# Performance work log

Measured on AMD Instinct MI355X. Metric: run time of the kernel, lower is better.

Reference implementation:

```python
import jax, jax.numpy as jnp
import numpy as np

N = 100000
E = 500000
D_IN = 128
D_H = 128
MAX_ITERS = 3  # min(int(T=2.0)+1, 3); step weights all >= 0.5 so no early break


def setup_inputs() -> dict:
    key = jax.random.key(0)
    ks = jax.random.split(key, 7)
    node_feats = jax.random.normal(ks[0], (N, D_IN), dtype=jnp.float32)
    edge_index = jax.random.randint(ks[1], (2, E), 0, N, dtype=jnp.int64)
    init = lambda k, shp, fan: jax.random.normal(k, shp, dtype=jnp.float32) / np.float32(np.sqrt(fan))
    W_s = init(ks[2], (D_H, D_IN), D_IN)        # Linear(d_in, d_h, bias=False)
    W_pc = init(ks[3], (D_H, D_H), D_H)         # Linear(d_h, d_h, bias=False)
    W_edge = init(ks[4], (D_H, 2 * D_H), 2 * D_H)  # Linear(2*d_h, d_h, bias=False)
    W_gate_w = init(ks[5], (1, 2 * D_H), 2 * D_H)  # Linear(2*d_h, 1)
    W_gate_b = jnp.zeros((1,), jnp.float32)
    T = jnp.float32(2.0)  # learnable iteration-count parameter, init tree_iterations
    return dict(node_feats=node_feats, edge_index=edge_index, W_s=W_s, W_pc=W_pc,
                W_edge=W_edge, W_gate_w=W_gate_w, W_gate_b=W_gate_b, T=T)


def _step(h, p_idx, c_idx, W_pc, W_edge, W_gate_w, W_gate_b):
    h_p = h[p_idx]                                   # [E, d_h] gather
    h_c = h[c_idx]                                   # [E, d_h] gather
    ec = jnp.concatenate([h_p, h_c], axis=1)         # [E, 2*d_h]
    msg = ec @ W_edge.T                              # edge projection
    alpha = jax.nn.sigmoid(ec @ W_gate_w.T + W_gate_b)  # [E, 1] gate
    msg = msg * alpha
    # scatter_add into both endpoints (symmetric aggregation)
    agg = jnp.zeros_like(h).at[p_idx].add(msg).at[c_idx].add(msg)
    new_h = jax.nn.relu(agg @ W_pc.T + h)
    return new_h + h  # residual=True


def reference(node_feats, edge_index, W_s, W_pc, W_edge, W_gate_w, W_gate_b, T):
    p_idx, c_idx = edge_index[0], edge_index[1]
    h = node_feats @ W_s.T                           # [N, d_h]
    for step in range(MAX_ITERS):
        w = jax.nn.sigmoid(T - step)                 # learned step weight
        step_h = _step(h, p_idx, c_idx, W_pc, W_edge, W_gate_w, W_gate_b)
        h = h + w * (step_h - h)
    return h  # outputs['hidden'] (dropout is identity in eval)
```

## Files before the change

### kernel.cpp

```cpp
#include <hip/hip_runtime.h>
#include <cstdio>
#include <cstddef>

#define DH 128

typedef _Float16 f16;
typedef __attribute__((ext_vector_type(8))) _Float16 f16x8;
typedef __attribute__((ext_vector_type(4))) _Float16 f16x4;
typedef __attribute__((ext_vector_type(2))) _Float16 f16x2;
typedef __attribute__((ext_vector_type(4))) float    f32x4;
typedef unsigned int u32;

__global__ __launch_bounds__(128) void wc_kernel(const float* __restrict__ Wpc,
                                                 const float* __restrict__ Wedge,
                                                 const float* __restrict__ Ws,
                                                 f16* __restrict__ Bg16,
                                                 f16* __restrict__ Ws16)
{
    int o = blockIdx.x;
    int k = threadIdx.x;
    if (o < 256) {
        int orow = o & 127;
        int col  = (o < 128) ? k : (128 + k);
        float acc = 0.f;
        for (int m = 0; m < 128; ++m)
            acc += Wpc[orow * 128 + m] * Wedge[m * 256 + col];
        Bg16[o * 128 + k] = (f16)acc;
    } else {
        int row = o - 256;
        Ws16[row * 128 + k] = (f16)Ws[row * 128 + k];
    }
}

__global__ __launch_bounds__(256) void prep_k(const int* __restrict__ idx,
                                              int* __restrict__ cnt, int twoE,
                                              const float* __restrict__ x,
                                              f16* __restrict__ x16, int n4)
{
    const int stride = gridDim.x * blockDim.x;
    const int mx = (twoE > n4) ? twoE : n4;
    for (int i = blockIdx.x * blockDim.x + threadIdx.x; i < mx; i += stride) {
        if (i < twoE) atomicAdd(cnt + idx[i], 1);
        if (i < n4) {
            float4 v = ((const float4*)x)[i];
            f16x2 a = {(f16)v.x, (f16)v.y};
            f16x2 b = {(f16)v.z, (f16)v.w};
            ((f16x2*)x16)[2 * i]     = a;
            ((f16x2*)x16)[2 * i + 1] = b;
        }
    }
}

template<int OUT, bool WF32, bool WF16, bool FUSES>
__global__ __launch_bounds__(256) void mfma_gemm_t(const f16* __restrict__ A16,
                                                   const f16* __restrict__ B16,
                                                   float* __restrict__ Cf,
                                                   f16* __restrict__ Ch,
                                                   const float* __restrict__ wg,
                                                   float* __restrict__ s,
                                                   int M)
{
    const int lane = threadIdx.x & 63;
    const int row0 = blockIdx.x * 128 + (threadIdx.x >> 6) * 32;
    const int r = lane & 15, kg = lane >> 4;

    const int mA = row0 + r,      mB = row0 + 16 + r;
    const bool okA = (mA < M),    okB = (mB < M);
    const int arA = okA ? mA : M - 1, arB = okB ? mB : M - 1;
    const f16x8* ApA = (const f16x8*)(A16 + (size_t)arA * 128 + kg * 8);
    const f16x8* ApB = (const f16x8*)(A16 + (size_t)arB * 128 + kg * 8);
    f16x8 a0 = ApA[0], a1 = ApA[4], a2 = ApA[8], a3 = ApA[12];
    f16x8 e0 = ApB[0], e1 = ApB[4], e2 = ApB[8], e3 = ApB[12];

    float spA0 = 0.f, spA1 = 0.f, spB0 = 0.f, spB1 = 0.f;

    for (int ct = 0; ct < OUT / 16; ++ct) {
        const f16x8* Bp = (const f16x8*)(B16 + (size_t)(ct * 16 + r) * 128 + kg * 8);
        f16x8 b0 = Bp[0], b1 = Bp[4], b2 = Bp[8], b3 = Bp[12];
        f32x4 acc0 = {0.f,0.f,0.f,0.f}, acc1 = {0.f,0.f,0.f,0.f};
        f32x4 acc2 = {0.f,0.f,0.f,0.f}, acc3 = {0.f,0.f,0.f,0.f};
        acc0 = __builtin_amdgcn_mfma_f32_16x16x32_f16(b0, a0, acc0, 0, 0, 0);
        acc2 = __builtin_amdgcn_mfma_f32_16x16x32_f16(b0, e0, acc2, 0, 0, 0);
        acc1 = __builtin_amdgcn_mfma_f32_16x16x32_f16(b2, a2, acc1, 0, 0, 0);
        acc3 = __builtin_amdgcn_mfma_f32_16x16x32_f16(b2, e2, acc3, 0, 0, 0);
        acc0 = __builtin_amdgcn_mfma_f32_16x16x32_f16(b1, a1, acc0, 0, 0, 0);
        acc2 = __builtin_amdgcn_mfma_f32_16x16x32_f16(b1, e1, acc2, 0, 0, 0);
        acc1 = __builtin_amdgcn_mfma_f32_16x16x32_f16(b3, a3, acc1, 0, 0, 0);
        acc3 = __builtin_amdgcn_mfma_f32_16x16x32_f16(b3, e3, acc3, 0, 0, 0);

        const int o0 = ct * 16 + kg * 4;
        float vA0 = acc0[0]+acc1[0], vA1 = acc0[1]+acc1[1];
        float vA2 = acc0[2]+acc1[2], vA3 = acc0[3]+acc1[3];
        float vB0 = acc2[0]+acc3[0], vB1 = acc2[1]+acc3[1];
        float vB2 = acc2[2]+acc3[2], vB3 = acc2[3]+acc3[3];
        if (okA) {
            if constexpr (WF32)
                *(float4*)(Cf + (size_t)mA * OUT + o0) = make_float4(vA0, vA1, vA2, vA3);
            if constexpr (WF16) {
                f16x4 hv = {(f16)vA0, (f16)vA1, (f16)vA2, (f16)vA3};
                *(f16x4*)(Ch + (size_t)mA * OUT + o0) = hv;
            }
        }
        if (okB) {
            if constexpr (WF32)
                *(float4*)(Cf + (size_t)mB * OUT + o0) = make_float4(vB0, vB1, vB2, vB3);
            if constexpr (WF16) {
                f16x4 hv = {(f16)vB0, (f16)vB1, (f16)vB2, (f16)vB3};
                *(f16x4*)(Ch + (size_t)mB * OUT + o0) = hv;
            }
        }
        if constexpr (FUSES) {
            float w0 = wg[o0], w1 = wg[o0+1], w2 = wg[o0+2], w3 = wg[o0+3];
            float u0 = wg[128+o0], u1 = wg[128+o0+1], u2 = wg[128+o0+2], u3 = wg[128+o0+3];
            spA0 += vA0*w0 + vA1*w1 + vA2*w2 + vA3*w3;
            spA1 += vA0*u0 + vA1*u1 + vA2*u2 + vA3*u3;
            spB0 += vB0*w0 + vB1*w1 + vB2*w2 + vB3*w3;
            spB1 += vB0*u0 + vB1*u1 + vB2*u2 + vB3*u3;
        }
    }
    if constexpr (FUSES) {
        spA0 += __shfl_xor(spA0, 16); spA0 += __shfl_xor(spA0, 32);
        spA1 += __shfl_xor(spA1, 16); spA1 += __shfl_xor(spA1, 32);
        spB0 += __shfl_xor(spB0, 16); spB0 += __shfl_xor(spB0, 32);
        spB1 += __shfl_xor(spB1, 16); spB1 += __shfl_xor(spB1, 32);
        if (kg == 0) {
            if (okA) *(float2*)(s + 2 * mA) = make_float2(spA0, spA1);
            if (okB) *(float2*)(s + 2 * mB) = make_float2(spB0, spB1);
        }
    }
}

#define SCAN_B 256
__global__ __launch_bounds__(SCAN_B) void scan1(const int* __restrict__ cnt,
                                                int* __restrict__ bsum, int Nn)
{
    __shared__ int sm[SCAN_B];
    int i = blockIdx.x * SCAN_B + threadIdx.x;
    sm[threadIdx.x] = (i < Nn) ? cnt[i] : 0;
    __syncthreads();
    for (int off = SCAN_B / 2; off > 0; off >>= 1) {
        if (threadIdx.x < off) sm[threadIdx.x] += sm[threadIdx.x + off];
        __syncthreads();
    }
    if (threadIdx.x == 0) bsum[blockIdx.x] = sm[0];
}

__global__ __launch_bounds__(1024) void scan2(int* __restrict__ bsum, int nb,
                                              int* __restrict__ totalOut)
{
    __shared__ int sm[1024];
    int t = threadIdx.x;
    sm[t] = (t < nb) ? bsum[t] : 0;
    __syncthreads();
    for (int off = 1; off < 1024; off <<= 1) {
        int u = (t >= off) ? sm[t - off] : 0;
        __syncthreads();
        sm[t] += u;
        __syncthreads();
    }
    if (t < nb) bsum[t] = (t == 0) ? 0 : sm[t - 1];
    if (t == nb - 1) *totalOut = sm[t];
}

__global__ __launch_bounds__(SCAN_B) void scan3(const int* __restrict__ cnt,
                                                const int* __restrict__ bsum,
                                                int* __restrict__ base,
                                                int* __restrict__ cursor, int Nn)
{
    __shared__ int sm[SCAN_B];
    int i = blockIdx.x * SCAN_B + threadIdx.x;
    int v = (i < Nn) ? cnt[i] : 0;
    sm[threadIdx.x] = v;
    __syncthreads();
    for (int off = 1; off < SCAN_B; off <<= 1) {
        int u = (threadIdx.x >= off) ? sm[threadIdx.x - off] : 0;
        __syncthreads();
        sm[threadIdx.x] += u;
        __syncthreads();
    }
    if (i < Nn) {
        int b = bsum[blockIdx.x] + sm[threadIdx.x] - v;
        base[i] = b;
        cursor[i] = b;
    }
}

__global__ __launch_bounds__(256) void fill_xcd(const int* __restrict__ idx,
                                                int* __restrict__ cursor,
                                                int* __restrict__ adjp,
                                                int E, int Nn)
{
    const int xcd  = blockIdx.x & 7;
    const int gblk = blockIdx.x >> 3;
    const int ngrp = gridDim.x >> 3;
    const int twoE = 2 * E;
    const int lo = xcd * Nn, hi = lo + Nn;
    for (int i = gblk * blockDim.x + threadIdx.x; i < twoE; i += ngrp * blockDim.x) {
        int node = idx[i];
        int n8 = node << 3;
        if (n8 < lo || n8 >= hi) continue;
        int side  = (i >= E);
        int e     = side ? i - E : i;
        int other = side ? idx[e] : idx[E + e];
        int pos = atomicAdd(cursor + node, 1);
        adjp[pos] = other | (side << 31);
    }
}

template<bool LAST>
__global__ __launch_bounds__(256) void agg4(const f16* __restrict__ g16,
                                            const int* __restrict__ adjp,
                                            const int* __restrict__ base,
                                            const float* __restrict__ sIn,
                                            float* __restrict__ sOut,
                                            float* __restrict__ h,
                                            f16* __restrict__ h16,
                                            const float* __restrict__ wg,
                                            const float* __restrict__ gbp,
                                            const float* __restrict__ Tp,
                                            float stepf, int Nn)
{
    const int lane = threadIdx.x & 63;
    const int n = (blockIdx.x * blockDim.x + threadIdx.x) >> 6;
    if (n >= Nn) return;
    const float gb = gbp[0];
    const float w  = 1.f / (1.f + expf(-(Tp[0] - stepf)));
    const int b0 = base[n], b1 = base[n + 1];
    const float s1n = sIn[2 * n], s2n = sIn[2 * n + 1];
    const int sub = lane >> 5;
    const int d0  = (lane & 31) << 2;

    f16x4 o1 = *(const f16x4*)(g16 + (size_t)n * 256 + d0);
    f16x4 o2 = *(const f16x4*)(g16 + (size_t)n * 256 + 128 + d0);
    float4 hv = *(const float4*)(h + (size_t)n * DH + d0);

    f16x2 accLo = {(f16)0.f, (f16)0.f};
    f16x2 accHi = {(f16)0.f, (f16)0.f};
    float aPl = 0.f, aCl = 0.f;

    union V4 { f16x4 v; f16x2 h2[2]; };
    union AU { u32 w; f16x2 h; unsigned short us[2]; };

    for (int c0 = b0; c0 < b1; c0 += 64) {
        const int m = (b1 - c0 < 64) ? (b1 - c0) : 64;
        int meta = adjp[c0 + ((lane < m) ? lane : (m - 1))];
        int other = meta & 0x7FFFFFFF;
        int side  = ((unsigned)meta) >> 31;
        int eoff  = (other << 8) | ((side ^ 1) << 7);
        float sv  = sIn[2 * other + (side ^ 1)];
        float aE  = 1.f / (1.f + expf(-((side ? s2n : s1n) + sv + gb)));
        if (lane >= m) aE = 0.f;
        aPl += side ? 0.f : aE;
        aCl += side ? aE : 0.f;

        AU apk;
        apk.h[0] = (f16)aE;
        apk.us[1] = apk.us[0];

        for (int j = 0; j < m; j += 16) {
            V4 gv[8]; u32 ap[8];
#pragma unroll
            for (int u = 0; u < 8; ++u) {
                int es = j + 2 * u + sub; es = (es < 63) ? es : 63;
                int eo = __shfl(eoff, es);
                ap[u]  = (u32)__shfl((int)apk.w, es);
                gv[u].v = *(const f16x4*)(g16 + (size_t)(unsigned)eo + d0);
            }
#pragma unroll
            for (int u = 0; u < 8; ++u) {
                AU aa; aa.w = ap[u];
                accLo += aa.h * gv[u].h2[0];
                accHi += aa.h * gv[u].h2[1];
            }
        }
    }

    float ax = (float)accLo[0], ay = (float)accLo[1];
    float az = (float)accHi[0], aw = (float)accHi[1];

    ax += __shfl_xor(ax, 32); ay += __shfl_xor(ay, 32);
    az += __shfl_xor(az, 32); aw += __shfl_xor(aw, 32);
    float aP = aPl, aC = aCl;
#pragma unroll
    for (int off = 32; off > 0; off >>= 1) {
        aP += __shfl_xor(aP, off);
        aC += __shfl_xor(aC, off);
    }
    ax += aP * (float)o1[0] + aC * (float)o2[0];
    ay += aP * (float)o1[1] + aC * (float)o2[1];
    az += aP * (float)o1[2] + aC * (float)o2[2];
    aw += aP * (float)o1[3] + aC * (float)o2[3];

    hv.x += w * fmaxf(ax + hv.x, 0.f);
    hv.y += w * fmaxf(ay + hv.y, 0.f);
    hv.z += w * fmaxf(az + hv.z, 0.f);
    hv.w += w * fmaxf(aw + hv.w, 0.f);

    float p0 = 0.f, p1 = 0.f;
    if (lane < 32) {
        *(float4*)(h + (size_t)n * DH + d0) = hv;
        if constexpr (!LAST) {
            f16x4 h2 = {(f16)hv.x, (f16)hv.y, (f16)hv.z, (f16)hv.w};
            *(f16x4*)(h16 + (size_t)n * DH + d0) = h2;
            float4 w0 = *(const float4*)(wg + d0);
            float4 w1 = *(const float4*)(wg + 128 + d0);
            p0 = hv.x*w0.x + hv.y*w0.y + hv.z*w0.z + hv.w*w0.w;
            p1 = hv.x*w1.x + hv.y*w1.y + hv.z*w1.z + hv.w*w1.w;
        }
    }
    if constexpr (!LAST) {
#pragma unroll
        for (int off = 16; off > 0; off >>= 1) {
            p0 += __shfl_xor(p0, off);
            p1 += __shfl_xor(p1, off);
        }
        if (lane == 0) *(float2*)(sOut + 2 * n) = make_float2(p0, p1);
    }
}

static inline size_t alignUp(size_t x) { return (x + 255) & ~(size_t)255; }

extern "C" void kernel_launch(void* const* d_in, const int* in_sizes, int n_in,
                              void* d_out, int out_size, void* d_ws, size_t ws_size,
                              hipStream_t stream)
{
    const float* x     = (const float*)d_in[0];
    const int*   idx   = (const int*)d_in[1];
    const float* Ws    = (const float*)d_in[2];
    const float* Wpc   = (const float*)d_in[3];
    const float* Wedge = (const float*)d_in[4];
    const float* Wg    = (const float*)d_in[5];
    const float* Wgb   = (const float*)d_in[6];
    const float* Tp    = (const float*)d_in[7];
    const int Nn = in_sizes[0] / DH;
    const int E  = in_sizes[1] / 2;
    float* h = (float*)d_out;

    const int nb = (Nn + SCAN_B - 1) / SCAN_B;
    if (nb > 1024) { fprintf(stderr, "kernel_launch: Nn too big for scan\n"); return; }

    size_t off = 0;
    char* wsb = (char*)d_ws;
    f16*   g16    = (f16*)  (wsb + off); off = alignUp(off + (size_t)Nn * 256 * 2);
    f16*   h16    = (f16*)  (wsb + off); off = alignUp(off + (size_t)Nn * DH * 2);
    f16*   x16    = (f16*)  (wsb + off); off = alignUp(off + (size_t)Nn * DH * 2);
    f16*   Ws16   = (f16*)  (wsb + off); off = alignUp(off + 128 * 128 * 2);
    f16*   Bg16   = (f16*)  (wsb + off); off = alignUp(off + 256 * 128 * 2);
    float* sA     = (float*)(wsb + off); off = alignUp(off + (size_t)Nn * 2 * 4);
    float* sB     = (float*)(wsb + off); off = alignUp(off + (size_t)Nn * 2 * 4);
    int*   cnt    = (int*)  (wsb + off); off = alignUp(off + (size_t)Nn * 4);
    int*   base   = (int*)  (wsb + off); off = alignUp(off + (size_t)(Nn + 1) * 4);
    int*   cursor = (int*)  (wsb + off); off = alignUp(off + (size_t)Nn * 4);
    int*   bsum   = (int*)  (wsb + off); off = alignUp(off + 1024 * 4);
    int*   adjp   = (int*)  (wsb + off); off = alignUp(off + (size_t)(2 * E) * 4);
    if (off > ws_size) {
        fprintf(stderr, "kernel_launch: ws too small (%zu < %zu)\n", ws_size, off);
        return;
    }

    hipMemsetAsync(cnt, 0, (size_t)Nn * 4, stream);
    prep_k<<<dim3(2048), dim3(256), 0, stream>>>(idx, cnt, 2 * E, x, x16, Nn * DH / 4);
    scan1<<<dim3(nb), dim3(SCAN_B), 0, stream>>>(cnt, bsum, Nn);
    scan2<<<dim3(1), dim3(1024), 0, stream>>>(bsum, nb, base + Nn);
    scan3<<<dim3(nb), dim3(SCAN_B), 0, stream>>>(cnt, bsum, base, cursor, Nn);
    fill_xcd<<<dim3(1280), dim3(256), 0, stream>>>(idx, cursor, adjp, E, Nn);

    wc_kernel<<<dim3(384), dim3(128), 0, stream>>>(Wpc, Wedge, Ws, Bg16, Ws16);
    mfma_gemm_t<128, true, true, true>
        <<<dim3((Nn + 127) / 128), dim3(256), 0, stream>>>(x16, Ws16, h, h16, Wg, sA, Nn);

    const int aggBlocks = (Nn * 64 + 255) / 256;
    float* sCur = sA; float* sNxt = sB;
    for (int step = 0; step < 3; ++step) {
        mfma_gemm_t<256, false, true, false>
            <<<dim3((Nn + 127) / 128), dim3(256), 0, stream>>>(h16, Bg16, nullptr, g16,
                                                               nullptr, nullptr, Nn);
        if (step < 2)
            agg4<false><<<dim3(aggBlocks), dim3(256), 0, stream>>>(g16, adjp, base, sCur,
                                                                   sNxt, h, h16, Wg, Wgb,
                                                                   Tp, (float)step, Nn);
        else
            agg4<true><<<dim3(aggBlocks), dim3(256), 0, stream>>>(g16, adjp, base, sCur,
                                                                  sNxt, h, h16, Wg, Wgb,
                                                                  Tp, (float)step, Nn);
        float* t = sCur; sCur = sNxt; sNxt = t;
    }
}
```

Before: 462.1 us.

## Process two nodes per wavefront in aggregation and prefetch GEMM B tiles

The aggregation kernel now assigns one 32-lane half-wave per node instead of a full 64-lane wave per node, halving the grid. It iterates over neighbours in chunks of 32 with a wave-wide any() loop condition. The aim is to remove the idle half-wave and the cross-half reduction for low-degree nodes (average degree about 10). In exchange, divergence grows when the two nodes sharing a wave have different degrees, and index clamping is needed near the end of the adjacency array. Separately, the MFMA GEMM loads the next column tile's B fragments while the current tile's MFMAs run, to hide load latency.

```diff
diff --git a/kernel.cpp b/kernel.cpp
--- a/kernel.cpp
+++ b/kernel.cpp
@@ -74,9 +74,15 @@
 
     float spA0 = 0.f, spA1 = 0.f, spB0 = 0.f, spB1 = 0.f;
 
+    const f16x8* Bp = (const f16x8*)(B16 + (size_t)r * 128 + kg * 8);
+    f16x8 b0 = Bp[0], b1 = Bp[4], b2 = Bp[8], b3 = Bp[12];
+
     for (int ct = 0; ct < OUT / 16; ++ct) {
-        const f16x8* Bp = (const f16x8*)(B16 + (size_t)(ct * 16 + r) * 128 + kg * 8);
-        f16x8 b0 = Bp[0], b1 = Bp[4], b2 = Bp[8], b3 = Bp[12];
+        f16x8 nb0, nb1, nb2, nb3;
+        if (ct + 1 < OUT / 16) {
+            const f16x8* Bn = (const f16x8*)(B16 + (size_t)((ct + 1) * 16 + r) * 128 + kg * 8);
+            nb0 = Bn[0]; nb1 = Bn[4]; nb2 = Bn[8]; nb3 = Bn[12];
+        }
         f32x4 acc0 = {0.f,0.f,0.f,0.f}, acc1 = {0.f,0.f,0.f,0.f};
         f32x4 acc2 = {0.f,0.f,0.f,0.f}, acc3 = {0.f,0.f,0.f,0.f};
         acc0 = __builtin_amdgcn_mfma_f32_16x16x32_f16(b0, a0, acc0, 0, 0, 0);
@@ -117,6 +123,7 @@
             spB0 += vB0*w0 + vB1*w1 + vB2*w2 + vB3*w3;
             spB1 += vB0*u0 + vB1*u1 + vB2*u2 + vB3*u3;
         }
+        b0 = nb0; b1 = nb1; b2 = nb2; b3 = nb3;
     }
     if constexpr (FUSES) {
         spA0 += __shfl_xor(spA0, 16); spA0 += __shfl_xor(spA0, 32);
@@ -208,7 +215,7 @@
 }
 
 template<bool LAST>
-__global__ __launch_bounds__(256) void agg4(const f16* __restrict__ g16,
+__global__ __launch_bounds__(256) void agg6(const f16* __restrict__ g16,
                                             const int* __restrict__ adjp,
                                             const int* __restrict__ base,
                                             const float* __restrict__ sIn,
@@ -218,17 +225,21 @@
                                             const float* __restrict__ wg,
                                             const float* __restrict__ gbp,
                                             const float* __restrict__ Tp,
-                                            float stepf, int Nn)
+                                            float stepf, int Nn, int twoE)
 {
     const int lane = threadIdx.x & 63;
-    const int n = (blockIdx.x * blockDim.x + threadIdx.x) >> 6;
-    if (n >= Nn) return;
+    const int grp  = lane >> 5;
+    const int gl   = lane & 31;
+    const int wvid = (blockIdx.x * blockDim.x + threadIdx.x) >> 6;
+    int n = wvid * 2 + grp;
+    const bool nOK = (n < Nn);
+    if (n >= Nn) n = Nn - 1;
     const float gb = gbp[0];
     const float w  = 1.f / (1.f + expf(-(Tp[0] - stepf)));
     const int b0 = base[n], b1 = base[n + 1];
+    const int deg = b1 - b0;
     const float s1n = sIn[2 * n], s2n = sIn[2 * n + 1];
-    const int sub = lane >> 5;
-    const int d0  = (lane & 31) << 2;
+    const int d0 = gl << 2;
 
     f16x4 o1 = *(const f16x4*)(g16 + (size_t)n * 256 + d0);
     f16x4 o2 = *(const f16x4*)(g16 + (size_t)n * 256 + 128 + d0);
@@ -241,15 +252,20 @@
     union V4 { f16x4 v; f16x2 h2[2]; };
     union AU { u32 w; f16x2 h; unsigned short us[2]; };
 
-    for (int c0 = b0; c0 < b1; c0 += 64) {
-        const int m = (b1 - c0 < 64) ? (b1 - c0) : 64;
-        int meta = adjp[c0 + ((lane < m) ? lane : (m - 1))];
+    int t = 0;
+    while (__any(t * 32 < deg)) {
+        const int done = t * 32;
+        int m = deg - done; m = (m < 0) ? 0 : ((m > 32) ? 32 : m);
+        int midx = b0 + done + ((gl < m) ? gl : ((m > 0) ? m - 1 : 0));
+        midx = (midx < twoE - 1) ? midx : (twoE - 1);
+        midx = (midx > 0) ? midx : 0;
+        int meta  = adjp[midx];
         int other = meta & 0x7FFFFFFF;
         int side  = ((unsigned)meta) >> 31;
         int eoff  = (other << 8) | ((side ^ 1) << 7);
         float sv  = sIn[2 * other + (side ^ 1)];
         float aE  = 1.f / (1.f + expf(-((side ? s2n : s1n) + sv + gb)));
-        if (lane >= m) aE = 0.f;
+        if (gl >= m) aE = 0.f;
         aPl += side ? 0.f : aE;
         aCl += side ? aE : 0.f;
 
@@ -257,13 +273,14 @@
         apk.h[0] = (f16)aE;
         apk.us[1] = apk.us[0];
 
-        for (int j = 0; j < m; j += 16) {
+        const int sb = grp << 5;
+        for (int j = 0; j < m; j += 8) {
             V4 gv[8]; u32 ap[8];
 #pragma unroll
             for (int u = 0; u < 8; ++u) {
-                int es = j + 2 * u + sub; es = (es < 63) ? es : 63;
-                int eo = __shfl(eoff, es);
-                ap[u]  = (u32)__shfl((int)apk.w, es);
+                int es = j + u; es = (es < 31) ? es : 31;
+                int eo = __shfl(eoff, sb | es);
+                ap[u]  = (u32)__shfl((int)apk.w, sb | es);
                 gv[u].v = *(const f16x4*)(g16 + (size_t)(unsigned)eo + d0);
             }
 #pragma unroll
@@ -273,16 +290,15 @@
                 accHi += aa.h * gv[u].h2[1];
             }
         }
+        ++t;
     }
 
     float ax = (float)accLo[0], ay = (float)accLo[1];
     float az = (float)accHi[0], aw = (float)accHi[1];
 
-    ax += __shfl_xor(ax, 32); ay += __shfl_xor(ay, 32);
-    az += __shfl_xor(az, 32); aw += __shfl_xor(aw, 32);
     float aP = aPl, aC = aCl;
 #pragma unroll
-    for (int off = 32; off > 0; off >>= 1) {
+    for (int off = 16; off > 0; off >>= 1) {
         aP += __shfl_xor(aP, off);
         aC += __shfl_xor(aC, off);
     }
@@ -297,24 +313,24 @@
     hv.w += w * fmaxf(aw + hv.w, 0.f);
 
     float p0 = 0.f, p1 = 0.f;
-    if (lane < 32) {
+    if (nOK) {
         *(float4*)(h + (size_t)n * DH + d0) = hv;
         if constexpr (!LAST) {
             f16x4 h2 = {(f16)hv.x, (f16)hv.y, (f16)hv.z, (f16)hv.w};
             *(f16x4*)(h16 + (size_t)n * DH + d0) = h2;
-            float4 w0 = *(const float4*)(wg + d0);
-            float4 w1 = *(const float4*)(wg + 128 + d0);
-            p0 = hv.x*w0.x + hv.y*w0.y + hv.z*w0.z + hv.w*w0.w;
-            p1 = hv.x*w1.x + hv.y*w1.y + hv.z*w1.z + hv.w*w1.w;
         }
     }
     if constexpr (!LAST) {
+        float4 w0 = *(const float4*)(wg + d0);
+        float4 w1 = *(const float4*)(wg + 128 + d0);
+        p0 = hv.x*w0.x + hv.y*w0.y + hv.z*w0.z + hv.w*w0.w;
+        p1 = hv.x*w1.x + hv.y*w1.y + hv.z*w1.z + hv.w*w1.w;
 #pragma unroll
         for (int off = 16; off > 0; off >>= 1) {
             p0 += __shfl_xor(p0, off);
             p1 += __shfl_xor(p1, off);
         }
-        if (lane == 0) *(float2*)(sOut + 2 * n) = make_float2(p0, p1);
+        if (gl == 0 && nOK) *(float2*)(sOut + 2 * n) = make_float2(p0, p1);
     }
 }
 
@@ -352,7 +368,7 @@
     int*   base   = (int*)  (wsb + off); off = alignUp(off + (size_t)(Nn + 1) * 4);
     int*   cursor = (int*)  (wsb + off); off = alignUp(off + (size_t)Nn * 4);
     int*   bsum   = (int*)  (wsb + off); off = alignUp(off + 1024 * 4);
-    int*   adjp   = (int*)  (wsb + off); off = alignUp(off + (size_t)(2 * E) * 4);
+    int*   adjp   = (int*)  (wsb + off); off = alignUp(off + (size_t)(2 * E + 64) * 4);
     if (off > ws_size) {
         fprintf(stderr, "kernel_launch: ws too small (%zu < %zu)\n", ws_size, off);
         return;
@@ -369,20 +385,20 @@
     mfma_gemm_t<128, true, true, true>
         <<<dim3((Nn + 127) / 128), dim3(256), 0, stream>>>(x16, Ws16, h, h16, Wg, sA, Nn);
 
-    const int aggBlocks = (Nn * 64 + 255) / 256;
+    const int aggBlocks = (Nn * 32 + 255) / 256;
     float* sCur = sA; float* sNxt = sB;
     for (int step = 0; step < 3; ++step) {
         mfma_gemm_t<256, false, true, false>
             <<<dim3((Nn + 127) / 128), dim3(256), 0, stream>>>(h16, Bg16, nullptr, g16,
                                                                nullptr, nullptr, Nn);
         if (step < 2)
-            agg4<false><<<dim3(aggBlocks), dim3(256), 0, stream>>>(g16, adjp, base, sCur,
+            agg6<false><<<dim3(aggBlocks), dim3(256), 0, stream>>>(g16, adjp, base, sCur,
                                                                    sNxt, h, h16, Wg, Wgb,
-                                                                   Tp, (float)step, Nn);
+                                                                   Tp, (float)step, Nn, 2 * E);
         else
-            agg4<true><<<dim3(aggBlocks), dim3(256), 0, stream>>>(g16, adjp, base, sCur,
+            agg6<true><<<dim3(aggBlocks), dim3(256), 0, stream>>>(g16, adjp, base, sCur,
                                                                   sNxt, h, h16, Wg, Wgb,
-                                                                  Tp, (float)step, Nn);
+                                                                  Tp, (float)step, Nn, 2 * E);
         float* t = sCur; sCur = sNxt; sNxt = t;
     }
 }
```

Result: faster. 450.6 us (-2.5%).
